# Kernel optimization log

Measured on AMD Instinct MI355X. Metric: run time of the kernel, lower is better.

Reference implementation:

```python
import jax, jax.numpy as jnp
import numpy as np
import math

N = 32768
C = 128
K = 16
CHUNK = 2048
LN_EPS = float(C)  # original code calls torch.nn.LayerNorm(C, C): second positional arg is eps -> eps = 128.0 (faithful)


def knn_idx(coords):
    """Brute-force KNN on full coords [N,4] (matches knn_points(x_C, x_C, K=16)), chunked over queries."""
    def one_chunk(q):  # q: [CHUNK,4]
        d = jnp.sum((q[:, None, :] - coords[None, :, :]) ** 2, axis=-1)  # [CHUNK,N]
        return jax.lax.top_k(-d, K)[1]  # ascending distance (return_sorted=True)
    qs = coords.reshape(-1, CHUNK, coords.shape[-1])
    return jax.lax.map(one_chunk, qs).reshape(-1, K)  # [N,K]


def layer_norm(x, g, b):
    mu = jnp.mean(x, axis=-1, keepdims=True)
    var = jnp.mean((x - mu) ** 2, axis=-1, keepdims=True)
    return (x - mu) / jnp.sqrt(var + LN_EPS) * g + b


def self_attention(x_f, xyz_enc, new_feature, qw, qb, kw, kb, vw, vb):
    Q = x_f @ qw + qb                              # [N,C]
    nf = new_feature + xyz_enc                     # [N,K,C]
    Kt = nf @ kw + kb                              # [N,K,C]
    scores = jnp.einsum('nkd,nd->nk', Kt, Q) / math.sqrt(C)
    a = jax.nn.softmax(scores, axis=-1)            # [N,K]
    V = nf @ vw + vb                               # [N,K,C]
    return jnp.einsum('nk,nkd->nd', a, V)          # [N,C]


def setup_inputs() -> dict:
    key = jax.random.key(0)
    ks = jax.random.split(key, 22)
    xyz = jax.random.uniform(ks[0], (N, 3), dtype=jnp.float32) * 100.0
    coords = jnp.concatenate([jnp.zeros((N, 1), jnp.float32), xyz], axis=1)  # [N,4] batch col = 0
    feats = jax.random.normal(ks[1], (N, C), dtype=jnp.float32)
    s = 0.02
    def lin(k, din, dout):
        kw, kb = jax.random.split(k)
        return jax.random.normal(kw, (din, dout), jnp.float32) * s, jax.random.normal(kb, (dout,), jnp.float32) * s
    pos_w, pos_b = lin(ks[2], 3, C)
    pos1_w, pos1_b = lin(ks[3], 3, C)
    qw0, qb0 = lin(ks[4], C, C); kw0, kb0 = lin(ks[5], C, C); vw0, vb0 = lin(ks[6], C, C)
    qw1, qb1 = lin(ks[7], C, C); kw1, kb1 = lin(ks[8], C, C); vw1, vb1 = lin(ks[9], C, C)
    lin_w, lin_b = lin(ks[10], C, C)  # MinkowskiConvolution kernel_size=1 == pointwise linear
    return {
        'coords': coords, 'feats': feats,
        'pos_w': pos_w, 'pos_b': pos_b, 'pos1_w': pos1_w, 'pos1_b': pos1_b,
        'qw0': qw0, 'qb0': qb0, 'kw0': kw0, 'kb0': kb0, 'vw0': vw0, 'vb0': vb0,
        'qw1': qw1, 'qb1': qb1, 'kw1': kw1, 'kb1': kb1, 'vw1': vw1, 'vb1': vb1,
        'lin_w': lin_w, 'lin_b': lin_b,
        'g0': jnp.ones((C,), jnp.float32), 'be0': jnp.zeros((C,), jnp.float32),
        'g1': jnp.ones((C,), jnp.float32), 'be1': jnp.zeros((C,), jnp.float32),
    }


def reference(coords, feats, pos_w, pos_b, pos1_w, pos1_b,
              qw0, qb0, kw0, kb0, vw0, vb0,
              qw1, qb1, kw1, kb1, vw1, vb1,
              lin_w, lin_b, g0, be0, g1, be1):
    idx = knn_idx(coords)                           # [N,K]
    xyz = coords[:, 1:]                             # [N,3]
    new_xyz = xyz[:, None, :] - xyz[idx]            # [N,K,3] relative offsets
    # block 1
    xyz_enc = new_xyz @ pos_w + pos_b               # [N,K,C]
    nf = feats[idx]                                 # gather [N,K,C]
    o = self_attention(feats, xyz_enc, nf, qw0, qb0, kw0, kb0, vw0, vb0)
    # block 2: re-gather updated features with same idx
    nf1 = o[idx]
    xyz_enc1 = new_xyz @ pos1_w + pos1_b
    o = self_attention(o, xyz_enc1, nf1, qw1, qb1, kw1, kb1, vw1, vb1)
    # residual + LN, pointwise conv, residual + LN
    h = layer_norm(feats + o, g0, be0)
    h1 = h @ lin_w + lin_b
    return layer_norm(h + h1, g1, be1)
```

## Files before the change

### kernel.cpp

```cpp
#include <hip/hip_runtime.h>
#include <stdint.h>

#define NPT 32768

typedef unsigned int u32;
typedef unsigned short u16;
typedef unsigned long long u64;

typedef short v8s __attribute__((ext_vector_type(8)));
typedef float v4f __attribute__((ext_vector_type(4)));

__device__ __forceinline__ float b2f(u16 u) {
  union { u32 u; float f; } x; x.u = ((u32)u) << 16; return x.f;
}
__device__ __forceinline__ u16 f2b(float f) {
  union { float f; u32 u; } x; x.f = f;
  u32 u = x.u;
  return (u16)((u + 0x7fffu + ((u >> 16) & 1u)) >> 16);
}
__device__ __forceinline__ bool probe_f32(const void* coords) {
  return ((const u16*)coords)[1] == 0;
}
__device__ __forceinline__ float ldany(const void* p, long i, bool f32) {
  return f32 ? ((const float*)p)[i] : b2f(((const u16*)p)[i]);
}
__device__ __forceinline__ float wsum(float v) {
#pragma unroll
  for (int m = 1; m < 64; m <<= 1) v += __shfl_xor(v, m, 64);
  return v;
}
__device__ __forceinline__ u64 sx64(u64 v, int m) {
  int lo = __shfl_xor((int)(u32)v, m, 64);
  int hi = __shfl_xor((int)(u32)(v >> 32), m, 64);
  return ((u64)(u32)hi << 32) | (u32)lo;
}
__device__ __forceinline__ u64 bc64(u64 v, int src) {
  int lo = __shfl((int)(u32)v, src, 64);
  int hi = __shfl((int)(u32)(v >> 32), src, 64);
  return ((u64)(u32)hi << 32) | (u32)lo;
}
__device__ __forceinline__ float dp8(uint4 a, uint4 b) {
  float s = 0.f;
#pragma unroll
  for (int i = 0; i < 4; i++) {
    u32 ua = ((const u32*)&a)[i], ub = ((const u32*)&b)[i];
    s += b2f((u16)(ua & 0xffffu)) * b2f((u16)(ub & 0xffffu));
    s += b2f((u16)(ua >> 16)) * b2f((u16)(ub >> 16));
  }
  return s;
}

#define GC 16
#define GH 6.25f
#define GINV 0.16f
#define NCELL (GC * GC * GC)

__device__ __forceinline__ int cell1d(float v) {
  int c = (int)(v * GINV);
  return c > (GC - 1) ? (GC - 1) : (c < 0 ? 0 : c);
}

__global__ __launch_bounds__(256) void conv_coords(const void* __restrict__ coords,
                                                   float* __restrict__ cx, float* __restrict__ cy,
                                                   float* __restrict__ cz, int* __restrict__ cellStart) {
  const bool f32 = probe_f32(coords);
  int i = blockIdx.x * 256 + threadIdx.x;
  cx[i] = ldany(coords, (long)i * 4 + 1, f32);
  cy[i] = ldany(coords, (long)i * 4 + 2, f32);
  cz[i] = ldany(coords, (long)i * 4 + 3, f32);
  if (i <= NCELL) cellStart[i] = 0;
}

__global__ __launch_bounds__(256) void conv_featsS(const void* __restrict__ coords,
                                                   const void* __restrict__ feats,
                                                   const float4* __restrict__ sortedP,
                                                   u16* __restrict__ featsS) {
  const bool f32 = probe_f32(coords);
  long i = (long)blockIdx.x * 256 + threadIdx.x;
  int s = (int)(i >> 7), c = (int)(i & 127);
  long orig = (long)__float_as_int(sortedP[s].w);
  featsS[i] = f32 ? f2b(((const float*)feats)[orig * 128 + c]) : ((const u16*)feats)[orig * 128 + c];
}

__global__ __launch_bounds__(256) void grid_hist(const float* __restrict__ cx, const float* __restrict__ cy,
                                                 const float* __restrict__ cz, int* __restrict__ cellStart,
                                                 int* __restrict__ pcell) {
  int i = blockIdx.x * 256 + threadIdx.x;
  int c = (cell1d(cz[i]) * GC + cell1d(cy[i])) * GC + cell1d(cx[i]);
  pcell[i] = c;
  atomicAdd(&cellStart[c + 1], 1);
}

__global__ __launch_bounds__(256) void grid_scan(int* __restrict__ cellStart, int* __restrict__ cellPtr) {
  __shared__ int part[256];
  const int t = threadIdx.x;
  int local[16]; int s = 0;
#pragma unroll
  for (int i = 0; i < 16; i++) { local[i] = cellStart[1 + t * 16 + i]; s += local[i]; }
  part[t] = s;
  __syncthreads();
  for (int off = 1; off < 256; off <<= 1) {
    int v = (t >= off) ? part[t - off] : 0;
    __syncthreads();
    part[t] += v;
    __syncthreads();
  }
  int run = (t == 0) ? 0 : part[t - 1];
#pragma unroll
  for (int i = 0; i < 16; i++) {
    int c = t * 16 + i;
    cellPtr[c] = run;
    run += local[i];
    cellStart[c + 1] = run;
  }
}

__global__ __launch_bounds__(256) void grid_scatter(const float* __restrict__ cx, const float* __restrict__ cy,
                                                    const float* __restrict__ cz, const int* __restrict__ pcell,
                                                    int* __restrict__ cellPtr, float4* __restrict__ sortedP,
                                                    int* __restrict__ rank) {
  int i = blockIdx.x * 256 + threadIdx.x;
  int c = pcell[i];
  int pos = atomicAdd(&cellPtr[c], 1);
  sortedP[pos] = make_float4(cx[i], cy[i], cz[i], __int_as_float(i));
  rank[i] = pos;
}

__global__ __launch_bounds__(256) void knn_grid(const float4* __restrict__ sortedP,
                                                const int* __restrict__ cellStart,
                                                const int* __restrict__ rank,
                                                u16* __restrict__ idxout) {
  const int lane = threadIdx.x & 63;
  const int q = blockIdx.x * 4 + (threadIdx.x >> 6);
  const float4 p = sortedP[q];
  const float qx = p.x, qy = p.y, qz = p.z;
  const int qcx = cell1d(qx), qcy = cell1d(qy), qcz = cell1d(qz);

  u64 R = ~0ull;

  auto key_of = [&](int g) -> u64 {
    float4 sp = sortedP[g];
    float dx = __fsub_rn(qx, sp.x), dy = __fsub_rn(qy, sp.y), dzc = __fsub_rn(qz, sp.z);
    float d = __fadd_rn(__fadd_rn(__fmul_rn(dx, dx), __fmul_rn(dy, dy)), __fmul_rn(dzc, dzc));
    return ((u64)__float_as_uint(d) << 32) | (u32)__float_as_int(sp.w);
  };

  auto batch_merge = [&](u64 key) {
    u64 k15 = bc64(R, 15);
    if (__ballot(key < k15) == 0ull) return;
#pragma unroll
    for (int k = 2; k <= 64; k <<= 1) {
#pragma unroll
      for (int j = k >> 1; j > 0; j >>= 1) {
        u64 o = sx64(key, j);
        bool up = ((lane & k) == 0);
        bool lower = ((lane & j) == 0);
        u64 mn = key < o ? key : o;
        u64 mx = key < o ? o : key;
        key = (lower == up) ? mn : mx;
      }
    }
    u64 s = sx64(key, 15);
    u64 mn = R < s ? R : s;
#pragma unroll
    for (int j = 8; j > 0; j >>= 1) {
      u64 o = sx64(mn, j);
      bool lower = ((lane & j) == 0);
      u64 lo = mn < o ? mn : o;
      u64 hi = mn < o ? o : mn;
      mn = lower ? lo : hi;
    }
    R = mn;
  };

  auto scan_range_wave = [&](int s0, int s1) {
    for (int base = s0; base < s1; base += 64) {
      int g = base + lane;
      u64 key = (g < s1) ? key_of(g) : ~0ull;
      batch_merge(key);
    }
  };

  {
    const int rord[9] = { 4, 1, 3, 5, 7, 0, 2, 6, 8 };
    int rs[9], rl[9];
#pragma unroll
    for (int s_ = 0; s_ < 9; s_++) {
      int row = rord[s_];
      int dz = row / 3 - 1, dy = row % 3 - 1;
      int z = qcz + dz, y = qcy + dy;
      if (z < 0 || z > GC - 1 || y < 0 || y > GC - 1) { rs[s_] = 0; rl[s_] = 0; }
      else {
        int rb = (z * GC + y) * GC;
        int xlo = qcx - 1 < 0 ? 0 : qcx - 1;
        int xhi = qcx + 1 > GC - 1 ? GC - 1 : qcx + 1;
        int s = cellStart[rb + xlo], e = cellStart[rb + xhi + 1];
        rs[s_] = s; rl[s_] = e - s;
      }
    }
    int cum[10]; cum[0] = 0;
#pragma unroll
    for (int i = 0; i < 9; i++) cum[i + 1] = cum[i] + rl[i];
    int total = cum[9];
    for (int base = 0; base < total; base += 64) {
      int pp = base + lane;
      u64 key = ~0ull;
      if (pp < total) {
        int g = 0;
#pragma unroll
        for (int i = 0; i < 9; i++) {
          if (pp >= cum[i] && pp < cum[i + 1]) g = rs[i] + (pp - cum[i]);
        }
        key = key_of(g);
      }
      batch_merge(key);
    }
  }

  {
    u64 k15 = bc64(R, 15);
    float d15 = __uint_as_float((u32)(k15 >> 32));
    float b1 = GH * 1.0f;
    if (!(d15 < b1 * b1 * 0.998f)) {
      for (int r = 2; r < GC; ++r) {
        int zlo = qcz - r < 0 ? 0 : qcz - r, zhi = qcz + r > GC - 1 ? GC - 1 : qcz + r;
        for (int z = zlo; z <= zhi; ++z) {
          int adz = z - qcz; adz = adz < 0 ? -adz : adz;
          bool ez = (adz == r);
          int ylo = qcy - r < 0 ? 0 : qcy - r, yhi = qcy + r > GC - 1 ? GC - 1 : qcy + r;
          for (int y = ylo; y <= yhi; ++y) {
            int ady = y - qcy; ady = ady < 0 ? -ady : ady;
            bool ey = (ady == r);
            int rb = (z * GC + y) * GC;
            if (ez || ey) {
              int xlo = qcx - r < 0 ? 0 : qcx - r, xhi = qcx + r > GC - 1 ? GC - 1 : qcx + r;
              scan_range_wave(cellStart[rb + xlo], cellStart[rb + xhi + 1]);
            } else {
              int xm = qcx - r, xp = qcx + r;
              if (xm >= 0) scan_range_wave(cellStart[rb + xm], cellStart[rb + xm + 1]);
              if (xp <= GC - 1) scan_range_wave(cellStart[rb + xp], cellStart[rb + xp + 1]);
            }
          }
        }
        k15 = bc64(R, 15);
        d15 = __uint_as_float((u32)(k15 >> 32));
        float bound = GH * (float)r;
        if (d15 < bound * bound * 0.998f) break;
      }
    }
  }

  if (lane < 16) idxout[(size_t)q * 16 + lane] = (u16)rank[(int)(u32)R];
}

__global__ __launch_bounds__(256) void prep_tables(
    const void* coords,
    const void* pw0, const void* pb0, const void* kw0, const void* kb0, const void* vw0, const void* vb0,
    const void* pw1, const void* pb1, const void* kw1, const void* kb1, const void* vw1, const void* vb1,
    float* __restrict__ tbl) {
  const bool f32 = probe_f32(coords);
  const int lane = threadIdx.x & 63;
  const int o = blockIdx.x * 4 + (threadIdx.x >> 6);
  const int l = o >> 10;
  const int rem = o & 1023;
  const void* PW = l ? pw1 : pw0;
  const void* PB = l ? pb1 : pb0;
  const void* KW = l ? kw1 : kw0;
  const void* KB = l ? kb1 : kb0;
  const void* VW = l ? vw1 : vw0;
  const void* VB = l ? vb1 : vb0;
  float acc, extra = 0.f;
  if (rem < 768) {
    bool isV = rem >= 384;
    int r2 = isV ? rem - 384 : rem;
    int i = r2 >> 7, c = r2 & 127;
    const void* W = isV ? VW : KW;
    acc = ldany(PW, i * 128 + lane, f32) * ldany(W, (long)lane * 128 + c, f32)
        + ldany(PW, i * 128 + lane + 64, f32) * ldany(W, (long)(lane + 64) * 128 + c, f32);
  } else {
    bool isV = rem >= 896;
    int c = rem & 127;
    const void* W = isV ? VW : KW;
    const void* B = isV ? VB : KB;
    acc = ldany(PB, lane, f32) * ldany(W, (long)lane * 128 + c, f32)
        + ldany(PB, lane + 64, f32) * ldany(W, (long)(lane + 64) * 128 + c, f32);
    extra = ldany(B, c, f32);
  }
  acc = wsum(acc) + extra;
  if (lane == 0) tbl[l * 1024 + rem] = acc;
}

__global__ __launch_bounds__(256) void prep_bfrag_all(const void* __restrict__ coords,
                                                      const void* __restrict__ qw0, const void* __restrict__ kw0,
                                                      const void* __restrict__ vw0, const void* __restrict__ qw1,
                                                      const void* __restrict__ kw1, const void* __restrict__ vw1,
                                                      const void* __restrict__ linw, u16* __restrict__ Bf0,
                                                      u16* __restrict__ Bf1, u16* __restrict__ BfL) {
  const bool f32 = probe_f32(coords);
  int tid = blockIdx.x * 256 + threadIdx.x;
  const void *w0, *w1, *w2; u16* out; int t;
  if (tid < 49152) { t = tid; w0 = qw0; w1 = kw0; w2 = vw0; out = Bf0; }
  else if (tid < 98304) { t = tid - 49152; w0 = qw1; w1 = kw1; w2 = vw1; out = Bf1; }
  else { t = tid - 98304; w0 = linw; w1 = linw; w2 = linw; out = BfL; }
  int j = t & 7, lane = (t >> 3) & 63, kq = (t >> 9) & 3, tile = t >> 11;
  int k = kq * 32 + ((lane >> 4) << 3) + j;
  int col = tile * 16 + (lane & 15);
  const void* w = (col < 128) ? w0 : ((col < 256) ? w1 : w2);
  long off = (long)k * 128 + (col & 127);
  out[t] = f32 ? f2b(((const float*)w)[off]) : ((const u16*)w)[off];
}

__global__ __launch_bounds__(256) void gemm_kernel(const void* __restrict__ coords,
                                                   const u16* __restrict__ A, const u16* __restrict__ Bf,
                                                   const void* __restrict__ bias, u16* __restrict__ Qb,
                                                   u16* __restrict__ KVb, float* __restrict__ outF,
                                                   int mode, int ntiles) {
  const bool f32 = probe_f32(coords);
  const int lane = threadIdx.x & 63;
  const int wave = threadIdx.x >> 6;
  const int r0 = blockIdx.x * 64 + wave * 16;
  const int quad = lane >> 4, lr = lane & 15;
  v8s a[4];
#pragma unroll
  for (int kq = 0; kq < 4; kq++) {
    union { uint4 u; v8s s; } c;
    c.u = *(const uint4*)(A + (size_t)(r0 + lr) * 128 + kq * 32 + quad * 8);
    a[kq] = c.s;
  }
  for (int tile = 0; tile < ntiles; ++tile) {
    v4f acc = { 0.f, 0.f, 0.f, 0.f };
#pragma unroll
    for (int kq = 0; kq < 4; kq++) {
      union { uint4 u; v8s s; } c;
      c.u = *(const uint4*)(Bf + ((size_t)(tile * 4 + kq) * 64 + lane) * 8);
      acc = __builtin_amdgcn_mfma_f32_16x16x32_bf16(a[kq], c.s, acc, 0, 0, 0);
    }
    int col = tile * 16 + lr;
    if (mode == 0) {
      if (col < 128) {
        float bb = ldany(bias, col, f32);
#pragma unroll
        for (int r = 0; r < 4; r++) Qb[(size_t)(r0 + quad * 4 + r) * 128 + col] = f2b(acc[r] + bb);
      } else {
#pragma unroll
        for (int r = 0; r < 4; r++) KVb[(size_t)(r0 + quad * 4 + r) * 256 + (col - 128)] = f2b(acc[r]);
      }
    } else {
      float bb = ldany(bias, col, f32);
#pragma unroll
      for (int r = 0; r < 4; r++) outF[(size_t)(r0 + quad * 4 + r) * 128 + col] = acc[r] + bb;
    }
  }
}

__global__ __launch_bounds__(256) void attn_kernel(const void* __restrict__ coordsRaw,
                                                   const float4* __restrict__ sortedP,
                                                   const u16* __restrict__ idx,
                                                   const u16* __restrict__ Qb, const u16* __restrict__ KVb,
                                                   const float* __restrict__ tbl, const void* __restrict__ feats,
                                                   const void* __restrict__ g, const void* __restrict__ be,
                                                   u16* __restrict__ outB, int mode) {
  const int lane = threadIdx.x & 63;
  const int n = blockIdx.x * 4 + (threadIdx.x >> 6);
  const int c0 = 2 * lane;
  const int k = lane & 15;
  const int quad = lane >> 4;
  const float4 P = sortedP[n];

  u32 qu = *(const u32*)(Qb + (size_t)n * 128 + c0);
  const float q0 = b2f((u16)(qu & 0xffffu)), q1 = b2f((u16)(qu >> 16));
  float p0 = tbl[c0] * q0 + tbl[c0 + 1] * q1;
  float p1 = tbl[128 + c0] * q0 + tbl[128 + c0 + 1] * q1;
  float p2 = tbl[256 + c0] * q0 + tbl[256 + c0 + 1] * q1;
  float p3 = tbl[768 + c0] * q0 + tbl[768 + c0 + 1] * q1;
#pragma unroll
  for (int m = 1; m < 64; m <<= 1) {
    p0 += __shfl_xor(p0, m, 64);
    p1 += __shfl_xor(p1, m, 64);
    p2 += __shfl_xor(p2, m, 64);
    p3 += __shfl_xor(p3, m, 64);
  }

  const int j = idx[(size_t)n * 16 + k];
  const float4 Pj = sortedP[j];
  const float nx = P.x - Pj.x, ny = P.y - Pj.y, nz = P.z - Pj.z;
  const u16* qrow = Qb + (size_t)n * 128 + quad * 32;
  const u16* krow = KVb + (size_t)j * 256 + quad * 32;
  uint4 qa = *(const uint4*)(qrow), qb2 = *(const uint4*)(qrow + 8);
  uint4 qc = *(const uint4*)(qrow + 16), qd = *(const uint4*)(qrow + 24);
  uint4 ka = *(const uint4*)(krow), kb2 = *(const uint4*)(krow + 8);
  uint4 kc = *(const uint4*)(krow + 16), kd = *(const uint4*)(krow + 24);
  float s = dp8(qa, ka) + dp8(qb2, kb2) + dp8(qc, kc) + dp8(qd, kd);
  s += __shfl_xor(s, 16, 64);
  s += __shfl_xor(s, 32, 64);
  float sc = (s + nx * p0 + ny * p1 + nz * p2 + p3) * 0.08838834764831845f;

  float mx = sc;
#pragma unroll
  for (int m = 1; m < 16; m <<= 1) mx = fmaxf(mx, __shfl_xor(mx, m, 64));
  float e = expf(sc - mx);
  float ssum = e;
#pragma unroll
  for (int m = 1; m < 16; m <<= 1) ssum += __shfl_xor(ssum, m, 64);
  const float a = e / ssum;

  float sA = a, wx = a * nx, wy = a * ny, wz = a * nz;
#pragma unroll
  for (int m = 1; m < 16; m <<= 1) {
    sA += __shfl_xor(sA, m, 64);
    wx += __shfl_xor(wx, m, 64);
    wy += __shfl_xor(wy, m, 64);
    wz += __shfl_xor(wz, m, 64);
  }

  const int base = lane & 48;
  float a0 = 0.f, a1 = 0.f;
#pragma unroll
  for (int k2 = 0; k2 < 16; k2++) {
    float ak = __shfl(a, base + k2, 64);
    int jk = __shfl(j, base + k2, 64);
    u32 u = *(const u32*)(KVb + (size_t)jk * 256 + 128 + c0);
    a0 += ak * b2f((u16)(u & 0xffffu));
    a1 += ak * b2f((u16)(u >> 16));
  }
  float o0 = a0 + wx * tbl[384 + c0] + wy * tbl[512 + c0] + wz * tbl[640 + c0] + sA * tbl[896 + c0];
  float o1 = a1 + wx * tbl[384 + c0 + 1] + wy * tbl[512 + c0 + 1] + wz * tbl[640 + c0 + 1] + sA * tbl[896 + c0 + 1];
  if (mode == 1) {
    const bool f32 = probe_f32(coordsRaw);
    long orig = (long)__float_as_int(P.w);
    float x0 = ldany(feats, orig * 128 + c0, f32) + o0;
    float x1 = ldany(feats, orig * 128 + c0 + 1, f32) + o1;
    float mu = wsum(x0 + x1) * (1.f / 128.f);
    float d0 = x0 - mu, d1 = x1 - mu;
    float var = wsum(d0 * d0 + d1 * d1) * (1.f / 128.f);
    float rinv = 1.0f / sqrtf(var + 128.0f);
    o0 = d0 * rinv * ldany(g, c0, f32) + ldany(be, c0, f32);
    o1 = d1 * rinv * ldany(g, c0 + 1, f32) + ldany(be, c0 + 1, f32);
  }
  ((u32*)outB)[(size_t)n * 64 + lane] = (u32)f2b(o0) | ((u32)f2b(o1) << 16);
}

__global__ __launch_bounds__(256) void ln_final(const void* __restrict__ coords,
                                                const float4* __restrict__ sortedP,
                                                const u16* __restrict__ hB, const float* __restrict__ h1F,
                                                const void* __restrict__ g, const void* __restrict__ be,
                                                void* __restrict__ outAny) {
  const bool f32 = probe_f32(coords);
  const int lane = threadIdx.x & 63;
  const int n = blockIdx.x * 4 + (threadIdx.x >> 6);
  const int c0 = 2 * lane;
  u32 u = *(const u32*)(hB + (size_t)n * 128 + c0);
  float2 h1 = *(const float2*)(h1F + (size_t)n * 128 + c0);
  float x0 = b2f((u16)(u & 0xffffu)) + h1.x;
  float x1 = b2f((u16)(u >> 16)) + h1.y;
  float mu = wsum(x0 + x1) * (1.f / 128.f);
  float d0 = x0 - mu, d1 = x1 - mu;
  float var = wsum(d0 * d0 + d1 * d1) * (1.f / 128.f);
  float rinv = 1.0f / sqrtf(var + 128.0f);
  float y0 = d0 * rinv * ldany(g, c0, f32) + ldany(be, c0, f32);
  float y1 = d1 * rinv * ldany(g, c0 + 1, f32) + ldany(be, c0 + 1, f32);
  size_t orig = (size_t)__float_as_int(sortedP[n].w);
  if (f32) {
    *(float2*)((float*)outAny + orig * 128 + c0) = make_float2(y0, y1);
  } else {
    ((u32*)outAny)[orig * 64 + lane] = (u32)f2b(y0) | ((u32)f2b(y1) << 16);
  }
}

extern "C" void kernel_launch(void* const* d_in, const int* in_sizes, int n_in,
                              void* d_out, int out_size, void* d_ws, size_t ws_size,
                              hipStream_t stream) {
  (void)in_sizes; (void)n_in; (void)out_size; (void)ws_size;
  const void* coords = d_in[0];
  const void* feats = d_in[1];
  const void* pos_w = d_in[2];
  const void* pos_b = d_in[3];
  const void* pos1_w = d_in[4];
  const void* pos1_b = d_in[5];
  const void* qw0 = d_in[6];
  const void* qb0 = d_in[7];
  const void* kw0 = d_in[8];
  const void* kb0 = d_in[9];
  const void* vw0 = d_in[10];
  const void* vb0 = d_in[11];
  const void* qw1 = d_in[12];
  const void* qb1 = d_in[13];
  const void* kw1 = d_in[14];
  const void* kb1 = d_in[15];
  const void* vw1 = d_in[16];
  const void* vb1 = d_in[17];
  const void* lin_w = d_in[18];
  const void* lin_b = d_in[19];
  const void* g0 = d_in[20];
  const void* be0 = d_in[21];
  const void* g1 = d_in[22];
  const void* be1 = d_in[23];

  char* w = (char*)d_ws;
  u16* idxp = (u16*)(w + 0);
  float4* sortedP = (float4*)(w + 1048576);
  int* rank = (int*)(w + 1572864);
  float* cx = (float*)(w + 1703936);
  float* cy = (float*)(w + 1835008);
  float* cz = (float*)(w + 1966080);
  float* tbl = (float*)(w + 2097152);
  u16* Bf0 = (u16*)(w + 2105344);
  u16* Bf1 = (u16*)(w + 2203648);
  u16* BfL = (u16*)(w + 2301952);
  u16* featsS = (u16*)(w + 2334720);
  u16* oS = (u16*)(w + 10723328);
  u16* Qb = (u16*)(w + 19111936);
  u16* KVb = (u16*)(w + 27500544);
  int* cellStart = (int*)(w + 19111936);
  int* cellPtr = (int*)(w + 19132416);
  int* pcell = (int*)(w + 19148800);
  float* h1F = (float*)(w + 19111936);

  hipLaunchKernelGGL(conv_coords, dim3(128), dim3(256), 0, stream, coords, cx, cy, cz, cellStart);
  hipLaunchKernelGGL(prep_tables, dim3(512), dim3(256), 0, stream, coords,
                     pos_w, pos_b, kw0, kb0, vw0, vb0, pos1_w, pos1_b, kw1, kb1, vw1, vb1, tbl);
  hipLaunchKernelGGL(prep_bfrag_all, dim3(448), dim3(256), 0, stream, coords,
                     qw0, kw0, vw0, qw1, kw1, vw1, lin_w, Bf0, Bf1, BfL);

  hipLaunchKernelGGL(grid_hist, dim3(128), dim3(256), 0, stream, cx, cy, cz, cellStart, pcell);
  hipLaunchKernelGGL(grid_scan, dim3(1), dim3(256), 0, stream, cellStart, cellPtr);
  hipLaunchKernelGGL(grid_scatter, dim3(128), dim3(256), 0, stream, cx, cy, cz, pcell, cellPtr, sortedP, rank);
  hipLaunchKernelGGL(conv_featsS, dim3(16384), dim3(256), 0, stream, coords, feats, sortedP, featsS);
  hipLaunchKernelGGL(knn_grid, dim3(8192), dim3(256), 0, stream, sortedP, cellStart, rank, idxp);

  hipLaunchKernelGGL(gemm_kernel, dim3(512), dim3(256), 0, stream, coords, featsS, Bf0, qb0, Qb, KVb,
                     (float*)nullptr, 0, 24);
  hipLaunchKernelGGL(attn_kernel, dim3(8192), dim3(256), 0, stream, coords, sortedP, idxp, Qb, KVb, tbl,
                     (const void*)nullptr, (const void*)nullptr, (const void*)nullptr, oS, 0);
  hipLaunchKernelGGL(gemm_kernel, dim3(512), dim3(256), 0, stream, coords, oS, Bf1, qb1, Qb, KVb,
                     (float*)nullptr, 0, 24);
  hipLaunchKernelGGL(attn_kernel, dim3(8192), dim3(256), 0, stream, coords, sortedP, idxp, Qb, KVb, tbl + 1024,
                     feats, g0, be0, oS, 1);
  hipLaunchKernelGGL(gemm_kernel, dim3(512), dim3(256), 0, stream, coords, oS, BfL, lin_b,
                     (u16*)nullptr, (u16*)nullptr, h1F, 1, 8);
  hipLaunchKernelGGL(ln_final, dim3(8192), dim3(256), 0, stream, coords, sortedP, oS, h1F, g1, be1, d_out);
}
```

Before: 343.6 us.

## Add sparse insertion path to KNN merge and fuse coord conversion with histogram

In the KNN batch merge, when few candidates (at most 12) beat the current 16th-best key, each one is inserted into the sorted register list with a shuffle-up step instead of running the full 64-wide bitonic sort and merge. Separately, the coordinate conversion and the grid histogram become one kernel, and zeroing of cellStart moves into prep_tables, which removes one launch. The serial insertion loop adds per-candidate shuffles and can be slower when the candidate count sits near the threshold.

```diff
diff --git a/kernel.cpp b/kernel.cpp
--- a/kernel.cpp
+++ b/kernel.cpp
@@ -39,6 +39,11 @@
   int hi = __shfl((int)(u32)(v >> 32), src, 64);
   return ((u64)(u32)hi << 32) | (u32)lo;
 }
+__device__ __forceinline__ u64 up64(u64 v) {
+  int lo = __shfl_up((int)(u32)v, 1, 64);
+  int hi = __shfl_up((int)(u32)(v >> 32), 1, 64);
+  return ((u64)(u32)hi << 32) | (u32)lo;
+}
 __device__ __forceinline__ float dp8(uint4 a, uint4 b) {
   float s = 0.f;
 #pragma unroll
@@ -60,15 +65,19 @@
   return c > (GC - 1) ? (GC - 1) : (c < 0 ? 0 : c);
 }
 
-__global__ __launch_bounds__(256) void conv_coords(const void* __restrict__ coords,
-                                                   float* __restrict__ cx, float* __restrict__ cy,
-                                                   float* __restrict__ cz, int* __restrict__ cellStart) {
+__global__ __launch_bounds__(256) void conv_coords_hist(const void* __restrict__ coords,
+                                                        float* __restrict__ cx, float* __restrict__ cy,
+                                                        float* __restrict__ cz, int* __restrict__ cellStart,
+                                                        int* __restrict__ pcell) {
   const bool f32 = probe_f32(coords);
   int i = blockIdx.x * 256 + threadIdx.x;
-  cx[i] = ldany(coords, (long)i * 4 + 1, f32);
-  cy[i] = ldany(coords, (long)i * 4 + 2, f32);
-  cz[i] = ldany(coords, (long)i * 4 + 3, f32);
-  if (i <= NCELL) cellStart[i] = 0;
+  float x = ldany(coords, (long)i * 4 + 1, f32);
+  float y = ldany(coords, (long)i * 4 + 2, f32);
+  float z = ldany(coords, (long)i * 4 + 3, f32);
+  cx[i] = x; cy[i] = y; cz[i] = z;
+  int c = (cell1d(z) * GC + cell1d(y)) * GC + cell1d(x);
+  pcell[i] = c;
+  atomicAdd(&cellStart[c + 1], 1);
 }
 
 __global__ __launch_bounds__(256) void conv_featsS(const void* __restrict__ coords,
@@ -82,15 +91,6 @@
   featsS[i] = f32 ? f2b(((const float*)feats)[orig * 128 + c]) : ((const u16*)feats)[orig * 128 + c];
 }
 
-__global__ __launch_bounds__(256) void grid_hist(const float* __restrict__ cx, const float* __restrict__ cy,
-                                                 const float* __restrict__ cz, int* __restrict__ cellStart,
-                                                 int* __restrict__ pcell) {
-  int i = blockIdx.x * 256 + threadIdx.x;
-  int c = (cell1d(cz[i]) * GC + cell1d(cy[i])) * GC + cell1d(cx[i]);
-  pcell[i] = c;
-  atomicAdd(&cellStart[c + 1], 1);
-}
-
 __global__ __launch_bounds__(256) void grid_scan(int* __restrict__ cellStart, int* __restrict__ cellPtr) {
   __shared__ int part[256];
   const int t = threadIdx.x;
@@ -145,9 +145,26 @@
     return ((u64)__float_as_uint(d) << 32) | (u32)__float_as_int(sp.w);
   };
 
+  auto insert_one = [&](u64 kk) {
+    u64 prev = up64(R);
+    if (lane == 0) prev = 0ull;
+    R = (kk < R) ? ((kk >= prev) ? kk : prev) : R;
+  };
+
   auto batch_merge = [&](u64 key) {
     u64 k15 = bc64(R, 15);
-    if (__ballot(key < k15) == 0ull) return;
+    u64 mask = __ballot(key < k15);
+    if (mask == 0ull) return;
+    int pcount = __popcll(mask);
+    if (pcount <= 12) {
+      while (mask) {
+        int s = __ffsll((long long)mask) - 1;
+        mask &= mask - 1ull;
+        u64 kk = bc64(key, s);
+        if (kk < bc64(R, 15)) insert_one(kk);
+      }
+      return;
+    }
 #pragma unroll
     for (int k = 2; k <= 64; k <<= 1) {
 #pragma unroll
@@ -257,8 +274,10 @@
     const void* coords,
     const void* pw0, const void* pb0, const void* kw0, const void* kb0, const void* vw0, const void* vb0,
     const void* pw1, const void* pb1, const void* kw1, const void* kb1, const void* vw1, const void* vb1,
-    float* __restrict__ tbl) {
+    float* __restrict__ tbl, int* __restrict__ cellStart) {
   const bool f32 = probe_f32(coords);
+  const int tid = blockIdx.x * 256 + threadIdx.x;
+  if (tid <= NCELL) cellStart[tid] = 0;
   const int lane = threadIdx.x & 63;
   const int o = blockIdx.x * 4 + (threadIdx.x >> 6);
   const int l = o >> 10;
@@ -516,13 +535,12 @@
   int* pcell = (int*)(w + 19148800);
   float* h1F = (float*)(w + 19111936);
 
-  hipLaunchKernelGGL(conv_coords, dim3(128), dim3(256), 0, stream, coords, cx, cy, cz, cellStart);
   hipLaunchKernelGGL(prep_tables, dim3(512), dim3(256), 0, stream, coords,
-                     pos_w, pos_b, kw0, kb0, vw0, vb0, pos1_w, pos1_b, kw1, kb1, vw1, vb1, tbl);
+                     pos_w, pos_b, kw0, kb0, vw0, vb0, pos1_w, pos1_b, kw1, kb1, vw1, vb1, tbl, cellStart);
+  hipLaunchKernelGGL(conv_coords_hist, dim3(128), dim3(256), 0, stream, coords, cx, cy, cz, cellStart, pcell);
   hipLaunchKernelGGL(prep_bfrag_all, dim3(448), dim3(256), 0, stream, coords,
                      qw0, kw0, vw0, qw1, kw1, vw1, lin_w, Bf0, Bf1, BfL);
 
-  hipLaunchKernelGGL(grid_hist, dim3(128), dim3(256), 0, stream, cx, cy, cz, cellStart, pcell);
   hipLaunchKernelGGL(grid_scan, dim3(1), dim3(256), 0, stream, cellStart, cellPtr);
   hipLaunchKernelGGL(grid_scatter, dim3(128), dim3(256), 0, stream, cx, cy, cz, pcell, cellPtr, sortedP, rank);
   hipLaunchKernelGGL(conv_featsS, dim3(16384), dim3(256), 0, stream, coords, feats, sortedP, featsS);
```

Result: faster. 327.8 us (-4.6%).
